# Kernel tuning notes

Hardware: AMD Instinct MI355X
Metric: run time of the kernel (lower is better)

Reference implementation:

```python
import jax, jax.numpy as jnp
import numpy as np

B, N, K = 64, 512, 32   # batch, node_num, top_k
D = 64                  # dim == embed_dim == input_dim == out_channels
EPS = 1e-5
NEG_SLOPE = 0.2         # LeakyReLU slope in GraphLayer.message
NEG_INF = -1e9


def setup_inputs() -> dict:
    key = jax.random.key(0)
    ks = jax.random.split(key, 20)
    rn = lambda k, shp, s=1.0: jax.random.normal(k, shp, jnp.float32) * s
    return {
        "data": rn(ks[0], (B, N, D)),
        "org_edge_index": jax.random.randint(ks[1], (2, 1024), 0, N),
        "emb_table": rn(ks[2], (N, D)),                 # nn.Embedding(node_num, dim)
        "lin_W": rn(ks[3], (D, D), 1.0 / np.sqrt(D)),   # GraphLayer.lin (no bias)
        "att_i": rn(ks[4], (D,), 0.1),
        "att_j": rn(ks[5], (D,), 0.1),
        "att_em_i": rn(ks[6], (D,), 0.1),
        "att_em_j": rn(ks[7], (D,), 0.1),
        "gnn_bias": rn(ks[8], (D,), 0.1),
        "bn1_gamma": 1.0 + rn(ks[9], (D,), 0.1),
        "bn1_beta": rn(ks[10], (D,), 0.1),
        "bn1_mean": rn(ks[11], (D,), 0.1),
        "bn1_var": 0.5 + jax.random.uniform(ks[12], (D,), jnp.float32),
        "bno_gamma": 1.0 + rn(ks[13], (D,), 0.1),
        "bno_beta": rn(ks[14], (D,), 0.1),
        "bno_mean": rn(ks[15], (D,), 0.1),
        "bno_var": 0.5 + jax.random.uniform(ks[16], (D,), jnp.float32),
        "out_W": rn(ks[17], (1, D), 1.0 / np.sqrt(D)),  # OutLayer single Linear(dim,1)
        "out_b": rn(ks[18], (1,), 0.1),
    }


def _gdn_forward(data, emb_table, lin_W, att_i, att_j, att_em_i, att_em_j, gnn_bias,
                 bn1_gamma, bn1_beta, bn1_mean, bn1_var,
                 bno_gamma, bno_beta, bno_mean, bno_var, out_W, out_b):
    Bn, Nn, Fin = data.shape
    x = data.reshape(-1, Fin)                               # [B*N, Fin]

    # --- dynamic graph: cosine-sim topk on detached embedding ---
    w = jax.lax.stop_gradient(emb_table)                    # weights_arr = emb.detach()
    nrm = jnp.linalg.norm(w, axis=-1)
    cos = (w @ w.T) / (nrm[:, None] * nrm[None, :])         # [N, N]
    topk_idx = jax.lax.top_k(cos, K)[1]                     # [N, K]
    src0 = topk_idx.reshape(-1)                             # j (sources)
    dst0 = jnp.repeat(jnp.arange(Nn), K)                    # i (targets)
    valid0 = src0 != dst0                                   # remove_self_loops
    offs = (jnp.arange(Bn) * Nn)[:, None]
    src = (src0[None, :] + offs).reshape(-1)                # [B*N*K]
    dst = (dst0[None, :] + offs).reshape(-1)
    valid = jnp.tile(valid0, Bn)
    loops = jnp.arange(Bn * Nn)                             # add_self_loops
    src = jnp.concatenate([src, loops])
    dst = jnp.concatenate([dst, loops])
    valid = jnp.concatenate([valid, jnp.ones(Bn * Nn, bool)])

    # --- GraphLayer (heads=1, concat=False) ---
    xl = x @ lin_W.T                                        # [B*N, D]
    src_l = src % Nn                                        # embedding tiled over batch
    dst_l = dst % Nn
    a = (xl[dst] @ att_i + emb_table[dst_l] @ att_em_i
         + xl[src] @ att_j + emb_table[src_l] @ att_em_j)   # [E]
    a = jnp.where(a >= 0, a, NEG_SLOPE * a)                 # leaky_relu
    a = jnp.where(valid, a, NEG_INF)
    seg = Bn * Nn
    amax = jax.ops.segment_max(a, dst, num_segments=seg)    # stable softmax per target
    ex = jnp.where(valid, jnp.exp(a - amax[dst]), 0.0)
    denom = jax.ops.segment_sum(ex, dst, num_segments=seg)
    alpha = ex / denom[dst]                                 # [E]
    agg = jax.ops.segment_sum(xl[src] * alpha[:, None], dst, num_segments=seg) + gnn_bias

    # --- GNNLayer BN (eval) + relu ---
    h = (agg - bn1_mean) / jnp.sqrt(bn1_var + EPS) * bn1_gamma + bn1_beta
    h = jax.nn.relu(h).reshape(Bn, Nn, -1)

    # --- mul by node embedding, BN over channels (eval), relu, dropout(eval)=id ---
    h = h * emb_table[None]
    h = (h - bno_mean) / jnp.sqrt(bno_var + EPS) * bno_gamma + bno_beta
    h = jax.nn.relu(h)

    # --- OutLayer: single Linear(dim, 1) ---
    out = h @ out_W.T + out_b                               # [B, N, 1]
    return out.reshape(-1, Nn)                              # [B, N]


def reference(data, org_edge_index, emb_table, lin_W, att_i, att_j, att_em_i, att_em_j,
              gnn_bias, bn1_gamma, bn1_beta, bn1_mean, bn1_var,
              bno_gamma, bno_beta, bno_mean, bno_var, out_W, out_b):
    # org_edge_index is accepted but unused by GDN.forward (dynamic graph replaces it)
    del org_edge_index
    return _gdn_forward(data, emb_table, lin_W, att_i, att_j, att_em_i, att_em_j, gnn_bias,
                        bn1_gamma, bn1_beta, bn1_mean, bn1_var,
                        bno_gamma, bno_beta, bno_mean, bno_var, out_W, out_b)
```

## Files before the change

kernel.cpp:

```cpp
#include <hip/hip_runtime.h>
#include <hip/hip_bf16.h>
#include <math.h>

#define BB 64
#define NN 512
#define KK 32
#define DD 64
#define BN (BB*NN)
#define EPSC 1e-5f
#define NEG_SLOPE 0.2f
#define NEG_INF_A (-1e9f)

typedef unsigned long long ull;


__global__ void kA_cos(const float* __restrict__ emb, ull* __restrict__ keys) {
    __shared__ float4 As[256];
    __shared__ float4 Bs[1024];
    __shared__ float rsA[16];
    const int t = threadIdx.x;
    const int lane = t & 63;
    const int wave = t >> 6;
    const int bi = blockIdx.x >> 3;
    const int c0 = (blockIdx.x & 7) * 64;
    const float4* emb4 = (const float4*)emb;

    As[t] = emb4[bi*256 + t];
    Bs[t]       = emb4[c0*16 + t];
    Bs[t + 256] = emb4[c0*16 + t + 256];
    Bs[t + 512] = emb4[c0*16 + t + 512];
    Bs[t + 768] = emb4[c0*16 + t + 768];
    __syncthreads();

    if (wave == 0) {
        const int r = lane >> 2, qq = lane & 3;
        float ss = 0.f;
        #pragma unroll
        for (int m = 0; m < 4; ++m) {
            const float4 a = As[r*16 + qq*4 + m];
            ss += a.x*a.x + a.y*a.y + a.z*a.z + a.w*a.w;
        }
        ss += __shfl_xor(ss, 1);
        ss += __shfl_xor(ss, 2);
        if (qq == 0) rsA[r] = rsqrtf(ss);
    }

    float4 Wr[16];
    float ssW = 0.f;
    #pragma unroll
    for (int q = 0; q < 16; ++q) {
        Wr[q] = Bs[lane*16 + q];
        ssW += Wr[q].x*Wr[q].x + Wr[q].y*Wr[q].y + Wr[q].z*Wr[q].z + Wr[q].w*Wr[q].w;
    }
    const float rsW = rsqrtf(ssW);
    __syncthreads();

    #pragma unroll
    for (int r = 0; r < 4; ++r) {
        const int jr = wave*4 + r;
        float acc = 0.f;
        #pragma unroll
        for (int q = 0; q < 16; ++q) {
            const float4 a = As[jr*16 + q];
            const float4 w = Wr[q];
            acc += a.x*w.x + a.y*w.y + a.z*w.z + a.w*w.w;
        }
        const float c = acc * rsA[jr] * rsW;
        const int row = bi*16 + jr;
        const int col = c0 + lane;
        unsigned int u = __float_as_uint(c);
        u = (u & 0x80000000u) ? ~u : (u | 0x80000000u);
        keys[row*NN + col] = ((ull)u << 16) | (ull)(NN - 1 - col);
    }
}

__global__ void kB_rank(const ull* __restrict__ keys,
                        const float* __restrict__ emb,
                        const float* __restrict__ att_em_i,
                        const float* __restrict__ att_em_j,
                        const float* __restrict__ gnn_bias,
                        const float* __restrict__ g1, const float* __restrict__ b1,
                        const float* __restrict__ m1, const float* __restrict__ v1,
                        const float* __restrict__ go, const float* __restrict__ bo,
                        const float* __restrict__ mo, const float* __restrict__ vo,
                        int* __restrict__ topk,
                        float* __restrict__ ei, float* __restrict__ ej,
                        float* __restrict__ epi) {
    __shared__ ull ks[NN];
    const int i = blockIdx.x;
    const int t = threadIdx.x;
    ks[t] = keys[i*NN + t];

    if (t < DD) {
        const float e = emb[i*DD + t];
        float e1 = e * att_em_i[t];
        float e2 = e * att_em_j[t];
        #pragma unroll
        for (int m = 32; m > 0; m >>= 1) {
            e1 += __shfl_xor(e1, m);
            e2 += __shfl_xor(e2, m);
        }
        if (t == 0) { ei[i] = e1; ej[i] = e2; }
    }
    if (i == 0 && t >= 64 && t < 64 + DD) {
        const int d = t - 64;
        float s1 = g1[d] / sqrtf(v1[d] + EPSC);
        float B1 = (gnn_bias[d] - m1[d]) * s1 + b1[d];
        float so = go[d] / sqrtf(vo[d] + EPSC);
        float Bo = bo[d] - mo[d] * so;
        epi[d] = s1; epi[DD + d] = B1; epi[2*DD + d] = so; epi[3*DD + d] = Bo;
    }
    __syncthreads();
    const ull mykey = ks[t];
    int rank = 0;
    #pragma unroll 16
    for (int kk = 0; kk < NN; ++kk) rank += (ks[kk] > mykey) ? 1 : 0;
    if (rank < KK) topk[i*KK + rank] = t;
}

__global__ void k2_lin(const float* __restrict__ data,
                       const float* __restrict__ linW,
                       const float* __restrict__ att_i, const float* __restrict__ att_j,
                       const float* __restrict__ ei, const float* __restrict__ ej,
                       float* __restrict__ xl, float* __restrict__ si,
                       float* __restrict__ sj) {
    __shared__ float4 Ws[1024];
    __shared__ float4 xs[256];
    const int t = threadIdx.x;
    const int lane = t & 63;
    const int wave = t >> 6;
    const float4* W4 = (const float4*)linW;

    Ws[t]       = W4[t];
    Ws[t + 256] = W4[t + 256];
    Ws[t + 512] = W4[t + 512];
    Ws[t + 768] = W4[t + 768];
    xs[t] = ((const float4*)data)[blockIdx.x*256 + t];
    __syncthreads();

    float4 Wr[16];
    #pragma unroll
    for (int q = 0; q < 16; ++q) Wr[q] = Ws[lane*16 + q];

    const int r0 = wave * 4;
    float acc0 = 0.f, acc1 = 0.f, acc2 = 0.f, acc3 = 0.f;
    #pragma unroll
    for (int q = 0; q < 16; ++q) {
        const float4 w = Wr[q];
        const float4 x0 = xs[(r0+0)*16 + q];
        const float4 x1 = xs[(r0+1)*16 + q];
        const float4 x2 = xs[(r0+2)*16 + q];
        const float4 x3 = xs[(r0+3)*16 + q];
        acc0 += x0.x*w.x + x0.y*w.y + x0.z*w.z + x0.w*w.w;
        acc1 += x1.x*w.x + x1.y*w.y + x1.z*w.z + x1.w*w.w;
        acc2 += x2.x*w.x + x2.y*w.y + x2.z*w.z + x2.w*w.w;
        acc3 += x3.x*w.x + x3.y*w.y + x3.z*w.z + x3.w*w.w;
    }

    const int vbase = blockIdx.x*16 + r0;
    xl[(vbase+0)*DD + lane] = acc0;
    xl[(vbase+1)*DD + lane] = acc1;
    xl[(vbase+2)*DD + lane] = acc2;
    xl[(vbase+3)*DD + lane] = acc3;

    const float ai = att_i[lane];
    const float aj = att_j[lane];
    float accs[4] = {acc0, acc1, acc2, acc3};
    #pragma unroll
    for (int r = 0; r < 4; ++r) {
        float pi = accs[r] * ai;
        float pj = accs[r] * aj;
        #pragma unroll
        for (int m = 32; m > 0; m >>= 1) {
            pi += __shfl_xor(pi, m);
            pj += __shfl_xor(pj, m);
        }
        if (lane == 0) {
            const int v = vbase + r;
            si[v] = pi + ei[v & (NN-1)];
            sj[v] = pj + ej[v & (NN-1)];
        }
    }
}

__global__ void k3_agg(const float* __restrict__ xl, const float* __restrict__ si,
                       const float* __restrict__ sj, const int* __restrict__ topk,
                       const float* __restrict__ emb,
                       const float* __restrict__ epi,
                       const float* __restrict__ outW, const float* __restrict__ outb,
                       float* __restrict__ out) {
    const int t = threadIdx.x;
    const int lane = t & 63;
    const int wave = t >> 6;
    const int tgt = blockIdx.x * 4 + wave;
    const int b = tgt >> 9;
    const int i = tgt & (NN - 1);

    const bool isedge = (lane <= KK);
    int tk = i;
    bool valid = true;
    if (lane < KK) { tk = topk[i*KK + lane]; valid = (tk != i); }
    const int srcg = b * NN + tk;

    float a;
    if (isedge) {
        a = si[tgt] + sj[srcg];
        a = (a >= 0.f) ? a : NEG_SLOPE * a;
        if (!valid) a = NEG_INF_A;
    } else {
        a = -3.0e38f;
    }

    float amax = a;
    #pragma unroll
    for (int m = 32; m > 0; m >>= 1) amax = fmaxf(amax, __shfl_xor(amax, m));

    float ex = (isedge && valid) ? __expf(a - amax) : 0.f;
    float denom = ex;
    #pragma unroll
    for (int m = 32; m > 0; m >>= 1) denom += __shfl_xor(denom, m);
    const float alpha = ex * __builtin_amdgcn_rcpf(denom);

    const int c4 = lane & 15;
    const int e4 = lane >> 4;
    const float4* xl4 = (const float4*)xl;
    float4 acc = make_float4(0.f, 0.f, 0.f, 0.f);
    #pragma unroll
    for (int m = 0; m < 8; ++m) {
        const int kk = 4*m + e4;
        const float al = __shfl(alpha, kk);
        const int   sg = __shfl(srcg, kk);
        const float4 xv = xl4[sg*16 + c4];
        acc.x += al*xv.x; acc.y += al*xv.y; acc.z += al*xv.z; acc.w += al*xv.w;
    }
    {
        const float al = __shfl(alpha, KK);
        const int   sg = __shfl(srcg, KK);
        if (e4 == 0) {
            const float4 xv = xl4[sg*16 + c4];
            acc.x += al*xv.x; acc.y += al*xv.y; acc.z += al*xv.z; acc.w += al*xv.w;
        }
    }
    #pragma unroll
    for (int m = 16; m <= 32; m <<= 1) {
        acc.x += __shfl_xor(acc.x, m);
        acc.y += __shfl_xor(acc.y, m);
        acc.z += __shfl_xor(acc.z, m);
        acc.w += __shfl_xor(acc.w, m);
    }

    const float4* epi4 = (const float4*)epi;
    const float4 s1 = epi4[c4];
    const float4 B1 = epi4[16 + c4];
    const float4 so = epi4[32 + c4];
    const float4 Bo = epi4[48 + c4];
    const float4 em = ((const float4*)emb)[i*16 + c4];
    const float4 w4 = ((const float4*)outW)[c4];
    float4 h;
    h.x = fmaxf(acc.x*s1.x + B1.x, 0.f) * em.x;
    h.y = fmaxf(acc.y*s1.y + B1.y, 0.f) * em.y;
    h.z = fmaxf(acc.z*s1.z + B1.z, 0.f) * em.z;
    h.w = fmaxf(acc.w*s1.w + B1.w, 0.f) * em.w;
    h.x = fmaxf(h.x*so.x + Bo.x, 0.f);
    h.y = fmaxf(h.y*so.y + Bo.y, 0.f);
    h.z = fmaxf(h.z*so.z + Bo.z, 0.f);
    h.w = fmaxf(h.w*so.w + Bo.w, 0.f);
    float p = h.x*w4.x + h.y*w4.y + h.z*w4.z + h.w*w4.w;
    p += __shfl_xor(p, 1);
    p += __shfl_xor(p, 2);
    p += __shfl_xor(p, 4);
    p += __shfl_xor(p, 8);
    if (lane == 0) out[tgt] = p + outb[0];
}

extern "C" void kernel_launch(void* const* d_in, const int* in_sizes, int n_in,
                              void* d_out, int out_size, void* d_ws, size_t ws_size,
                              hipStream_t stream) {
    (void)in_sizes; (void)n_in; (void)out_size; (void)ws_size;
    const float* data   = (const float*)d_in[0];
    const float* emb    = (const float*)d_in[2];
    const float* linW   = (const float*)d_in[3];
    const float* att_i  = (const float*)d_in[4];
    const float* att_j  = (const float*)d_in[5];
    const float* attemi = (const float*)d_in[6];
    const float* attemj = (const float*)d_in[7];
    const float* gbias  = (const float*)d_in[8];
    const float* g1     = (const float*)d_in[9];
    const float* b1     = (const float*)d_in[10];
    const float* m1     = (const float*)d_in[11];
    const float* v1     = (const float*)d_in[12];
    const float* go     = (const float*)d_in[13];
    const float* bo     = (const float*)d_in[14];
    const float* mo     = (const float*)d_in[15];
    const float* vo     = (const float*)d_in[16];
    const float* outW   = (const float*)d_in[17];
    const float* outb   = (const float*)d_in[18];
    float* out = (float*)d_out;

    char* ws = (char*)d_ws;
    float* ei   = (float*)(ws + 0);
    float* ej   = (float*)(ws + 4096);
    float* epi  = (float*)(ws + 8192);
    int*   topk = (int*)  (ws + 16384);
    float* si   = (float*)(ws + 81920);
    float* sj   = (float*)(ws + 212992);
    float* xl   = (float*)(ws + 344064);
    ull*   keys = (ull*)  (ws + 344064);

    kA_cos<<<256, 256, 0, stream>>>(emb, keys);
    kB_rank<<<NN, NN, 0, stream>>>(keys, emb, attemi, attemj, gbias,
                                   g1, b1, m1, v1, go, bo, mo, vo,
                                   topk, ei, ej, epi);
    k2_lin<<<BN/16, 256, 0, stream>>>(data, linW, att_i, att_j, ei, ej,
                                      xl, si, sj);
    k3_agg<<<BN/4, 256, 0, stream>>>(xl, si, sj, topk, emb, epi,
                                     outW, outb, out);
}
```

Measured before the change: 153.6 us.

## Swizzle LDS weight tiles, remap agg blocks per XCD, batch gather loads

Stores the 64x64 weight/embedding tiles in LDS with an XOR swizzle so the per-lane row reads (lane*16+q) no longer bank-conflict in the cosine and linear kernels. The aggregation kernel remaps block IDs so that each XCD handles whole batches, which keeps the gathered source rows of one batch in a single XCD's L2. It also issues all nine gather loads before accumulating, exposing memory-level parallelism. The costs are extra index arithmetic and more registers held by the hoisted loads.

```diff
diff --git a/kernel.cpp b/kernel.cpp
--- a/kernel.cpp
+++ b/kernel.cpp
@@ -26,10 +26,12 @@
     const float4* emb4 = (const float4*)emb;
 
     As[t] = emb4[bi*256 + t];
-    Bs[t]       = emb4[c0*16 + t];
-    Bs[t + 256] = emb4[c0*16 + t + 256];
-    Bs[t + 512] = emb4[c0*16 + t + 512];
-    Bs[t + 768] = emb4[c0*16 + t + 768];
+    #pragma unroll
+    for (int p = 0; p < 4; ++p) {
+        const int idx = t + 256*p;
+        const int r = idx >> 4, q = idx & 15;
+        Bs[(r<<4) | (q ^ (r & 15))] = emb4[c0*16 + idx];
+    }
     __syncthreads();
 
     if (wave == 0) {
@@ -49,7 +51,7 @@
     float ssW = 0.f;
     #pragma unroll
     for (int q = 0; q < 16; ++q) {
-        Wr[q] = Bs[lane*16 + q];
+        Wr[q] = Bs[(lane<<4) | (q ^ (lane & 15))];
         ssW += Wr[q].x*Wr[q].x + Wr[q].y*Wr[q].y + Wr[q].z*Wr[q].z + Wr[q].w*Wr[q].w;
     }
     const float rsW = rsqrtf(ssW);
@@ -131,16 +133,18 @@
     const int wave = t >> 6;
     const float4* W4 = (const float4*)linW;
 
-    Ws[t]       = W4[t];
-    Ws[t + 256] = W4[t + 256];
-    Ws[t + 512] = W4[t + 512];
-    Ws[t + 768] = W4[t + 768];
+    #pragma unroll
+    for (int p = 0; p < 4; ++p) {
+        const int idx = t + 256*p;
+        const int r = idx >> 4, q = idx & 15;
+        Ws[(r<<4) | (q ^ (r & 15))] = W4[idx];
+    }
     xs[t] = ((const float4*)data)[blockIdx.x*256 + t];
     __syncthreads();
 
     float4 Wr[16];
     #pragma unroll
-    for (int q = 0; q < 16; ++q) Wr[q] = Ws[lane*16 + q];
+    for (int q = 0; q < 16; ++q) Wr[q] = Ws[(lane<<4) | (q ^ (lane & 15))];
 
     const int r0 = wave * 4;
     float acc0 = 0.f, acc1 = 0.f, acc2 = 0.f, acc3 = 0.f;
@@ -192,9 +196,12 @@
     const int t = threadIdx.x;
     const int lane = t & 63;
     const int wave = t >> 6;
-    const int tgt = blockIdx.x * 4 + wave;
-    const int b = tgt >> 9;
-    const int i = tgt & (NN - 1);
+    const int bid = blockIdx.x;
+    const int xcd = bid & 7;
+    const int ixc = bid >> 3;
+    const int b   = xcd + 8 * (ixc >> 7);
+    const int i   = ((ixc & 127) << 2) + wave;
+    const int tgt = b * NN + i;
 
     const bool isedge = (lane <= KK);
     int tk = i;
@@ -224,23 +231,31 @@
     const int c4 = lane & 15;
     const int e4 = lane >> 4;
     const float4* xl4 = (const float4*)xl;
-    float4 acc = make_float4(0.f, 0.f, 0.f, 0.f);
+
+    float al[9];
+    int   off[9];
     #pragma unroll
     for (int m = 0; m < 8; ++m) {
         const int kk = 4*m + e4;
-        const float al = __shfl(alpha, kk);
-        const int   sg = __shfl(srcg, kk);
-        const float4 xv = xl4[sg*16 + c4];
-        acc.x += al*xv.x; acc.y += al*xv.y; acc.z += al*xv.z; acc.w += al*xv.w;
-    }
-    {
-        const float al = __shfl(alpha, KK);
-        const int   sg = __shfl(srcg, KK);
-        if (e4 == 0) {
-            const float4 xv = xl4[sg*16 + c4];
-            acc.x += al*xv.x; acc.y += al*xv.y; acc.z += al*xv.z; acc.w += al*xv.w;
-        }
-    }
+        al[m]  = __shfl(alpha, kk);
+        off[m] = __shfl(srcg, kk)*16 + c4;
+    }
+    const float alpha32 = __shfl(alpha, KK);
+    const int   srcg32  = __shfl(srcg, KK);
+    al[8]  = (e4 == 0) ? alpha32 : 0.f;
+    off[8] = srcg32*16 + c4;
+
+    float4 xv[9];
+    #pragma unroll
+    for (int m = 0; m < 9; ++m) xv[m] = xl4[off[m]];
+
+    float4 acc = make_float4(0.f, 0.f, 0.f, 0.f);
+    #pragma unroll
+    for (int m = 0; m < 9; ++m) {
+        acc.x += al[m]*xv[m].x; acc.y += al[m]*xv[m].y;
+        acc.z += al[m]*xv[m].z; acc.w += al[m]*xv[m].w;
+    }
+
     #pragma unroll
     for (int m = 16; m <= 32; m <<= 1) {
         acc.x += __shfl_xor(acc.x, m);
```

After: 137.0 us. 10.8% less time.
